# Optimization experiments

Measured on AMD Instinct MI355X. Metric: run time of the kernel, lower is better.

Reference implementation:

```python
import jax, jax.numpy as jnp
import numpy as np

N = 100_000      # nodes
E = 1_600_000    # edges (avg degree 16)
D = 64           # node feature dim
C = 2            # num_classes
K = 2            # propagation hops


def setup_inputs() -> dict:
    key = jax.random.key(0)
    k1, k2, k3 = jax.random.split(key, 3)
    x = jax.random.normal(k1, (N, D), dtype=jnp.float32)
    edge_index = jax.random.randint(k2, (2, E), 0, N, dtype=jnp.int64)
    W = jax.random.normal(k3, (C, D), dtype=jnp.float32) * 0.1  # torch Linear weight [out,in]
    b = jnp.zeros((C,), dtype=jnp.float32)
    return {"x": x, "edge_index": edge_index, "W": W, "b": b}


def reference(x, edge_index, W, b):
    n = x.shape[0]
    self_loop = jnp.arange(n, dtype=edge_index.dtype)
    row = jnp.concatenate([edge_index[0], self_loop])  # source
    col = jnp.concatenate([edge_index[1], self_loop])  # target
    # GCN symmetric normalization with self-loops (PyG gcn_norm)
    deg = jax.ops.segment_sum(jnp.ones(col.shape, dtype=x.dtype), col, num_segments=n)
    dinv = jnp.where(deg > 0, jax.lax.rsqrt(deg), 0.0)
    norm = dinv[row] * dinv[col]                      # [E+N]
    # K-hop propagation: x <- A_hat x
    for _ in range(K):
        x = jax.ops.segment_sum(norm[:, None] * x[row], col, num_segments=n)
    logits = x @ W.T + b                               # [N, C]
    return jax.nn.log_softmax(logits, axis=1)
```

## Files before the change

### kernel.cpp

```cpp
#include <hip/hip_runtime.h>
#include <hip/hip_bf16.h>
#include <math.h>


#define NODES 100000
#define EDGES 1600000
#define DIM 64

#define PBITS 12
#define PSIZE 4096
#define P_BUCKETS 25
#define CAP 131072
#define NSLICE 10
#define PART_BLOCKS 256
#define SEG (EDGES / PART_BLOCKS)
#define PAIRS (SEG / 2)

__global__ void init_kernel(const void* ei, int* mode, int* cursor) {
  int t = threadIdx.x;
  const int* p = (const int*)ei;
  unsigned long long ball = __ballot(p[2 * t + 1] == 0);
  if (t == 0) *mode = (ball == ~0ULL) ? 1 : 0;
  if (t < P_BUCKETS) cursor[t] = t * CAP;
}

__global__ void partition_kernel(const void* ei, const int* __restrict__ mode,
                                 int* __restrict__ cursor,
                                 int2* __restrict__ ecbuf) {
  __shared__ int lcnt[P_BUCKETS];
  __shared__ int lbase[P_BUCKETS];
  int t = threadIdx.x;
  int m = *mode;
  int pbase = blockIdx.x * PAIRS;

  if (t < P_BUCKETS) lcnt[t] = 0;
  __syncthreads();

  if (m) {
    const longlong2* cp =
        (const longlong2*)((const long long*)ei + EDGES) + pbase;
    for (int i = t; i < PAIRS; i += 256) {
      longlong2 v = cp[i];
      atomicAdd(&lcnt[((int)v.x) >> PBITS], 1);
      atomicAdd(&lcnt[((int)v.y) >> PBITS], 1);
    }
  } else {
    const int2* cp = (const int2*)((const int*)ei + EDGES) + pbase;
    for (int i = t; i < PAIRS; i += 256) {
      int2 v = cp[i];
      atomicAdd(&lcnt[v.x >> PBITS], 1);
      atomicAdd(&lcnt[v.y >> PBITS], 1);
    }
  }
  __syncthreads();
  if (t < P_BUCKETS) {
    lbase[t] = atomicAdd(&cursor[t], lcnt[t]);
    lcnt[t] = 0;
  }
  __syncthreads();

  if (m) {
    const longlong2* rp = (const longlong2*)ei + pbase;
    const longlong2* cp =
        (const longlong2*)((const long long*)ei + EDGES) + pbase;
    for (int i = t; i < PAIRS; i += 256) {
      longlong2 rv = rp[i];
      longlong2 cv = cp[i];
      int r0 = (int)rv.x, c0 = (int)cv.x;
      int b0 = c0 >> PBITS;
      int p0 = lbase[b0] + atomicAdd(&lcnt[b0], 1);
      if (p0 < (b0 + 1) * CAP) ecbuf[p0] = make_int2(r0, c0 & (PSIZE - 1));
      int r1 = (int)rv.y, c1 = (int)cv.y;
      int b1 = c1 >> PBITS;
      int p1 = lbase[b1] + atomicAdd(&lcnt[b1], 1);
      if (p1 < (b1 + 1) * CAP) ecbuf[p1] = make_int2(r1, c1 & (PSIZE - 1));
    }
  } else {
    const int2* rp = (const int2*)ei + pbase;
    const int2* cp = (const int2*)((const int*)ei + EDGES) + pbase;
    for (int i = t; i < PAIRS; i += 256) {
      int2 rv = rp[i];
      int2 cv = cp[i];
      int b0 = cv.x >> PBITS;
      int p0 = lbase[b0] + atomicAdd(&lcnt[b0], 1);
      if (p0 < (b0 + 1) * CAP) ecbuf[p0] = make_int2(rv.x, cv.x & (PSIZE - 1));
      int b1 = cv.y >> PBITS;
      int p1 = lbase[b1] + atomicAdd(&lcnt[b1], 1);
      if (p1 < (b1 + 1) * CAP) ecbuf[p1] = make_int2(rv.y, cv.y & (PSIZE - 1));
    }
  }
}

__global__ void deg_kernel(const int* __restrict__ cursor,
                           const int2* __restrict__ ecbuf,
                           float* __restrict__ dinv) {
  __shared__ int h[PSIZE];
  int p = blockIdx.x;
  for (int i = threadIdx.x; i < PSIZE; i += 1024) h[i] = 0;
  __syncthreads();
  int base = p * CAP;
  int cnt = min(cursor[p] - base, CAP);
  for (int e = threadIdx.x; e < cnt; e += 1024)
    atomicAdd(&h[ecbuf[base + e].y], 1);
  __syncthreads();
  int gbase = p << PBITS;
  for (int i = threadIdx.x; i < PSIZE; i += 1024) {
    int g = gbase + i;
    if (g < NODES) dinv[g] = rsqrtf((float)(h[i] + 1));
  }
}

__global__ void proj_kernel(const float* __restrict__ x,
                            const float* __restrict__ W,
                            const float* __restrict__ dinv,
                            float2* __restrict__ ts) {
  int wid = (blockIdx.x * (blockDim.x >> 6)) + (threadIdx.x >> 6);
  int d = threadIdx.x & 63;
  if (wid >= NODES) return;
  float xv = x[(size_t)wid * DIM + d];
  float p0 = xv * W[d];
  float p1 = xv * W[DIM + d];
#pragma unroll
  for (int off = 32; off >= 1; off >>= 1) {
    p0 += __shfl_xor(p0, off, 64);
    p1 += __shfl_xor(p1, off, 64);
  }
  if (d == 0) {
    float di = dinv[wid];
    float2 t;
    t.x = di * p0;
    t.y = di * p1;
    ts[wid] = t;
  }
}

__global__ void hop_kernel(const int* __restrict__ cursor,
                           const int2* __restrict__ ecbuf,
                           const float2* __restrict__ feat,
                           float2* __restrict__ hpart) {
  __shared__ float lx[PSIZE];
  __shared__ float ly[PSIZE];
  int p = blockIdx.x / NSLICE, s = blockIdx.x % NSLICE;
  for (int i = threadIdx.x; i < PSIZE; i += 512) {
    lx[i] = 0.f;
    ly[i] = 0.f;
  }
  __syncthreads();
  int base = p * CAP;
  int cnt = min(cursor[p] - base, CAP);
  int per = (cnt + NSLICE - 1) / NSLICE;
  int beg = base + s * per;
  int end = min(base + cnt, beg + per);
  for (int e = beg + threadIdx.x; e < end; e += 512) {
    int2 ec = ecbuf[e];
    float2 v = feat[ec.x];
    atomicAdd(&lx[ec.y], v.x);
    atomicAdd(&ly[ec.y], v.y);
  }
  __syncthreads();
  float2* outp = hpart + (size_t)blockIdx.x * PSIZE;
  for (int i = threadIdx.x; i < PSIZE; i += 512) {
    float2 o;
    o.x = lx[i];
    o.y = ly[i];
    outp[i] = o;
  }
}

__global__ void merge1_kernel(const float2* __restrict__ hpart,
                              const float2* __restrict__ ts,
                              const float* __restrict__ dinv,
                              float2* __restrict__ z) {
  int i = blockIdx.x * blockDim.x + threadIdx.x;
  if (i >= NODES) return;
  int p = i >> PBITS, l = i & (PSIZE - 1);
  float2 t0 = ts[i];
  float ax = t0.x, ay = t0.y;
#pragma unroll
  for (int s = 0; s < NSLICE; s++) {
    float2 v = hpart[(size_t)(p * NSLICE + s) * PSIZE + l];
    ax += v.x;
    ay += v.y;
  }
  float di = dinv[i];
  float sc = di * di;
  float2 o;
  o.x = sc * ax;
  o.y = sc * ay;
  z[i] = o;
}

__global__ void merge2_kernel(const float2* __restrict__ hpart,
                              const float2* __restrict__ z,
                              const float* __restrict__ dinv,
                              const float* __restrict__ bias,
                              float2* __restrict__ out) {
  int i = blockIdx.x * blockDim.x + threadIdx.x;
  if (i >= NODES) return;
  int p = i >> PBITS, l = i & (PSIZE - 1);
  float2 z0 = z[i];
  float ax = z0.x, ay = z0.y;
#pragma unroll
  for (int s = 0; s < NSLICE; s++) {
    float2 v = hpart[(size_t)(p * NSLICE + s) * PSIZE + l];
    ax += v.x;
    ay += v.y;
  }
  float di = dinv[i];
  float l0 = di * ax + bias[0];
  float l1 = di * ay + bias[1];
  float m = fmaxf(l0, l1);
  float ls = m + logf(expf(l0 - m) + expf(l1 - m));
  float2 o;
  o.x = l0 - ls;
  o.y = l1 - ls;
  out[i] = o;
}

extern "C" void kernel_launch(void* const* d_in, const int* in_sizes, int n_in,
                              void* d_out, int out_size, void* d_ws,
                              size_t ws_size, hipStream_t stream) {
  const float* x = (const float*)d_in[0];
  const void* ei = d_in[1];
  const float* W = (const float*)d_in[2];
  const float* b = (const float*)d_in[3];
  float2* out = (float2*)d_out;

  char* w = (char*)d_ws;
  size_t off = 0;
  auto alloc = [&](size_t bytes) -> char* {
    char* p = w + off;
    off += (bytes + 255) & ~(size_t)255;
    return p;
  };
  int* mode = (int*)alloc(sizeof(int));
  int* cursor = (int*)alloc(P_BUCKETS * sizeof(int));
  int2* ecbuf = (int2*)alloc((size_t)P_BUCKETS * CAP * sizeof(int2));
  float* dinv = (float*)alloc(NODES * sizeof(float));
  float2* ts = (float2*)alloc(NODES * sizeof(float2));
  float2* z = (float2*)alloc(NODES * sizeof(float2));
  float2* hpart =
      (float2*)alloc((size_t)P_BUCKETS * NSLICE * PSIZE * sizeof(float2));
  (void)ws_size;

  const int NGRID = (NODES + 255) / 256;

  init_kernel<<<1, 64, 0, stream>>>(ei, mode, cursor);
  partition_kernel<<<PART_BLOCKS, 256, 0, stream>>>(ei, mode, cursor, ecbuf);
  deg_kernel<<<P_BUCKETS, 1024, 0, stream>>>(cursor, ecbuf, dinv);

  const int WPB = 256 / 64;
  proj_kernel<<<(NODES + WPB - 1) / WPB, 256, 0, stream>>>(x, W, dinv, ts);

  hop_kernel<<<P_BUCKETS * NSLICE, 512, 0, stream>>>(cursor, ecbuf, ts, hpart);
  merge1_kernel<<<NGRID, 256, 0, stream>>>(hpart, ts, dinv, z);
  hop_kernel<<<P_BUCKETS * NSLICE, 512, 0, stream>>>(cursor, ecbuf, z, hpart);
  merge2_kernel<<<NGRID, 256, 0, stream>>>(hpart, z, dinv, b, out);
}
```

Baseline: 177.4 us.

## Fuse GCN pipeline into single cooperative persistent kernel with grid syncs

Replaces the eight separate launches (init, partition, degree, projection, two hops, two merges) with one cooperative kernel of 250 blocks of 1024 threads. The stages are separated by grid-wide syncs. Degree counting is split across slices with a per-slice histogram merge, and the projection uses 16-lane groups with float4 loads. The goal is to remove launch gaps and tail effects between small kernels. The cost is grid-sync overhead, and the partition phase now runs with fewer, larger blocks. The old multi-kernel path is kept as a fallback if the cooperative launch fails.

```diff
diff --git a/kernel.cpp b/kernel.cpp
--- a/kernel.cpp
+++ b/kernel.cpp
@@ -1,6 +1,8 @@
 #include <hip/hip_runtime.h>
-#include <hip/hip_bf16.h>
+#include <hip/hip_cooperative_groups.h>
 #include <math.h>
+
+namespace cg = cooperative_groups;
 
 
 #define NODES 100000
@@ -12,11 +14,209 @@
 #define P_BUCKETS 25
 #define CAP 131072
 #define NSLICE 10
-#define PART_BLOCKS 256
-#define SEG (EDGES / PART_BLOCKS)
-#define PAIRS (SEG / 2)
-
-__global__ void init_kernel(const void* ei, int* mode, int* cursor) {
+#define NBLOCKS (P_BUCKETS * NSLICE)
+#define NT 1024
+#define NPB (NODES / NBLOCKS)
+#define EPB (EDGES / NBLOCKS)
+#define PPB (EPB / 2)
+
+__global__ __launch_bounds__(NT) void gcn_all(
+    const void* __restrict__ ei, const float* __restrict__ x,
+    const float* __restrict__ W, const float* __restrict__ bias,
+    float2* __restrict__ out, int* __restrict__ mode, int* __restrict__ cursor,
+    int2* __restrict__ ecbuf, int* __restrict__ dpart,
+    float* __restrict__ dinv, float2* __restrict__ ts, float2* __restrict__ z,
+    float2* __restrict__ hpart) {
+  cg::grid_group grid = cg::this_grid();
+  __shared__ int shCnt[P_BUCKETS];
+  __shared__ int shBase[P_BUCKETS];
+  __shared__ int shHist[PSIZE];
+  __shared__ float shAx[PSIZE];
+  __shared__ float shAy[PSIZE];
+
+  const int b = blockIdx.x;
+  const int t = threadIdx.x;
+
+  if (b == 0) {
+    if (t < 64) {
+      const int* p = (const int*)ei;
+      unsigned long long ball = __ballot(p[2 * t + 1] == 0);
+      if (t == 0) *mode = (ball == ~0ULL) ? 1 : 0;
+    }
+    if (t < P_BUCKETS) cursor[t] = t * CAP;
+  }
+  grid.sync();
+
+  {
+    const int m = *mode;
+    if (t < P_BUCKETS) shCnt[t] = 0;
+    __syncthreads();
+    const int pbase = b * PPB;
+    if (m) {
+      const longlong2* cp =
+          (const longlong2*)((const long long*)ei + EDGES) + pbase;
+      for (int i = t; i < PPB; i += NT) {
+        longlong2 v = cp[i];
+        atomicAdd(&shCnt[((int)v.x) >> PBITS], 1);
+        atomicAdd(&shCnt[((int)v.y) >> PBITS], 1);
+      }
+    } else {
+      const int2* cp = (const int2*)((const int*)ei + EDGES) + pbase;
+      for (int i = t; i < PPB; i += NT) {
+        int2 v = cp[i];
+        atomicAdd(&shCnt[v.x >> PBITS], 1);
+        atomicAdd(&shCnt[v.y >> PBITS], 1);
+      }
+    }
+    __syncthreads();
+    if (t < P_BUCKETS) {
+      shBase[t] = atomicAdd(&cursor[t], shCnt[t]);
+      shCnt[t] = 0;
+    }
+    __syncthreads();
+    if (m) {
+      const longlong2* rp = (const longlong2*)ei + pbase;
+      const longlong2* cp =
+          (const longlong2*)((const long long*)ei + EDGES) + pbase;
+      for (int i = t; i < PPB; i += NT) {
+        longlong2 rv = rp[i];
+        longlong2 cv = cp[i];
+        int c0 = (int)cv.x, b0 = c0 >> PBITS;
+        int p0 = shBase[b0] + atomicAdd(&shCnt[b0], 1);
+        if (p0 < (b0 + 1) * CAP)
+          ecbuf[p0] = make_int2((int)rv.x, c0 & (PSIZE - 1));
+        int c1 = (int)cv.y, b1 = c1 >> PBITS;
+        int p1 = shBase[b1] + atomicAdd(&shCnt[b1], 1);
+        if (p1 < (b1 + 1) * CAP)
+          ecbuf[p1] = make_int2((int)rv.y, c1 & (PSIZE - 1));
+      }
+    } else {
+      const int2* rp = (const int2*)ei + pbase;
+      const int2* cp = (const int2*)((const int*)ei + EDGES) + pbase;
+      for (int i = t; i < PPB; i += NT) {
+        int2 rv = rp[i];
+        int2 cv = cp[i];
+        int b0 = cv.x >> PBITS;
+        int p0 = shBase[b0] + atomicAdd(&shCnt[b0], 1);
+        if (p0 < (b0 + 1) * CAP)
+          ecbuf[p0] = make_int2(rv.x, cv.x & (PSIZE - 1));
+        int b1 = cv.y >> PBITS;
+        int p1 = shBase[b1] + atomicAdd(&shCnt[b1], 1);
+        if (p1 < (b1 + 1) * CAP)
+          ecbuf[p1] = make_int2(rv.y, cv.y & (PSIZE - 1));
+      }
+    }
+  }
+  grid.sync();
+
+  const int pb = b / NSLICE, sl = b % NSLICE;
+  const int sbase = pb * CAP;
+  const int scnt = min(cursor[pb] - sbase, CAP);
+  const int sper = (scnt + NSLICE - 1) / NSLICE;
+  const int sbeg = sbase + sl * sper;
+  const int send = min(sbase + scnt, sbeg + sper);
+
+  {
+    for (int i = t; i < PSIZE; i += NT) shHist[i] = 0;
+    __syncthreads();
+    for (int e = sbeg + t; e < send; e += NT)
+      atomicAdd(&shHist[ecbuf[e].y], 1);
+    __syncthreads();
+    int* op = dpart + (size_t)b * PSIZE;
+    for (int i = t; i < PSIZE; i += NT) op[i] = shHist[i];
+  }
+  grid.sync();
+
+  {
+    const int nbase = b * NPB;
+    if (t < NPB) {
+      int i = nbase + t;
+      int p = i >> PBITS, l = i & (PSIZE - 1);
+      int d = 0;
+#pragma unroll
+      for (int s = 0; s < NSLICE; s++)
+        d += dpart[(size_t)(p * NSLICE + s) * PSIZE + l];
+      dinv[i] = rsqrtf((float)(d + 1));
+    }
+    __syncthreads();
+    const int wave = t >> 6, lane = t & 63;
+    const int g = lane >> 4, r = lane & 15;
+    for (int k = wave * 4; k < NPB; k += (NT / 64) * 4) {
+      int kk = k + g;
+      if (kk < NPB) {
+        int node = nbase + kk;
+        float4 xv = *(const float4*)&x[(size_t)node * DIM + r * 4];
+        float4 w0 = *(const float4*)&W[r * 4];
+        float4 w1 = *(const float4*)&W[DIM + r * 4];
+        float p0 = xv.x * w0.x + xv.y * w0.y + xv.z * w0.z + xv.w * w0.w;
+        float p1 = xv.x * w1.x + xv.y * w1.y + xv.z * w1.z + xv.w * w1.w;
+#pragma unroll
+        for (int off = 8; off >= 1; off >>= 1) {
+          p0 += __shfl_xor(p0, off, 16);
+          p1 += __shfl_xor(p1, off, 16);
+        }
+        if (r == 0) {
+          float di = dinv[node];
+          ts[node] = make_float2(di * p0, di * p1);
+        }
+      }
+    }
+  }
+  grid.sync();
+
+  for (int hop = 0; hop < 2; ++hop) {
+    const float2* feat = hop ? z : ts;
+    for (int i = t; i < PSIZE; i += NT) {
+      shAx[i] = 0.f;
+      shAy[i] = 0.f;
+    }
+    __syncthreads();
+    for (int e = sbeg + t; e < send; e += NT) {
+      int2 ec = ecbuf[e];
+      float2 v = feat[ec.x];
+      atomicAdd(&shAx[ec.y], v.x);
+      atomicAdd(&shAy[ec.y], v.y);
+    }
+    __syncthreads();
+    {
+      float2* op = hpart + (size_t)b * PSIZE;
+      for (int i = t; i < PSIZE; i += NT)
+        op[i] = make_float2(shAx[i], shAy[i]);
+    }
+    grid.sync();
+    const int nbase = b * NPB;
+    if (t < NPB) {
+      int i = nbase + t;
+      int p = i >> PBITS, l = i & (PSIZE - 1);
+      float2 self = hop ? z[i] : ts[i];
+      float ax = self.x, ay = self.y;
+#pragma unroll
+      for (int s = 0; s < NSLICE; s++) {
+        float2 v = hpart[(size_t)(p * NSLICE + s) * PSIZE + l];
+        ax += v.x;
+        ay += v.y;
+      }
+      float di = dinv[i];
+      if (hop == 0) {
+        float sc = di * di;
+        z[i] = make_float2(sc * ax, sc * ay);
+      } else {
+        float l0 = di * ax + bias[0];
+        float l1 = di * ay + bias[1];
+        float mm = fmaxf(l0, l1);
+        float ls = mm + logf(expf(l0 - mm) + expf(l1 - mm));
+        out[i] = make_float2(l0 - ls, l1 - ls);
+      }
+    }
+    if (hop == 0) grid.sync();
+  }
+}
+
+#define FPART_BLOCKS 256
+#define FSEG (EDGES / FPART_BLOCKS)
+#define FPAIRS (FSEG / 2)
+
+__global__ void fb_init(const void* ei, int* mode, int* cursor) {
   int t = threadIdx.x;
   const int* p = (const int*)ei;
   unsigned long long ball = __ballot(p[2 * t + 1] == 0);
@@ -24,29 +224,25 @@
   if (t < P_BUCKETS) cursor[t] = t * CAP;
 }
 
-__global__ void partition_kernel(const void* ei, const int* __restrict__ mode,
-                                 int* __restrict__ cursor,
-                                 int2* __restrict__ ecbuf) {
+__global__ void fb_partition(const void* ei, const int* __restrict__ mode,
+                             int* __restrict__ cursor, int2* __restrict__ ecbuf) {
   __shared__ int lcnt[P_BUCKETS];
   __shared__ int lbase[P_BUCKETS];
   int t = threadIdx.x;
   int m = *mode;
-  int pbase = blockIdx.x * PAIRS;
-
+  int pbase = blockIdx.x * FPAIRS;
   if (t < P_BUCKETS) lcnt[t] = 0;
   __syncthreads();
-
   if (m) {
-    const longlong2* cp =
-        (const longlong2*)((const long long*)ei + EDGES) + pbase;
-    for (int i = t; i < PAIRS; i += 256) {
+    const longlong2* cp = (const longlong2*)((const long long*)ei + EDGES) + pbase;
+    for (int i = t; i < FPAIRS; i += 256) {
       longlong2 v = cp[i];
       atomicAdd(&lcnt[((int)v.x) >> PBITS], 1);
       atomicAdd(&lcnt[((int)v.y) >> PBITS], 1);
     }
   } else {
     const int2* cp = (const int2*)((const int*)ei + EDGES) + pbase;
-    for (int i = t; i < PAIRS; i += 256) {
+    for (int i = t; i < FPAIRS; i += 256) {
       int2 v = cp[i];
       atomicAdd(&lcnt[v.x >> PBITS], 1);
       atomicAdd(&lcnt[v.y >> PBITS], 1);
@@ -58,27 +254,23 @@
     lcnt[t] = 0;
   }
   __syncthreads();
-
   if (m) {
     const longlong2* rp = (const longlong2*)ei + pbase;
-    const longlong2* cp =
-        (const longlong2*)((const long long*)ei + EDGES) + pbase;
-    for (int i = t; i < PAIRS; i += 256) {
+    const longlong2* cp = (const longlong2*)((const long long*)ei + EDGES) + pbase;
+    for (int i = t; i < FPAIRS; i += 256) {
       longlong2 rv = rp[i];
       longlong2 cv = cp[i];
-      int r0 = (int)rv.x, c0 = (int)cv.x;
-      int b0 = c0 >> PBITS;
+      int c0 = (int)cv.x, b0 = c0 >> PBITS;
       int p0 = lbase[b0] + atomicAdd(&lcnt[b0], 1);
-      if (p0 < (b0 + 1) * CAP) ecbuf[p0] = make_int2(r0, c0 & (PSIZE - 1));
-      int r1 = (int)rv.y, c1 = (int)cv.y;
-      int b1 = c1 >> PBITS;
+      if (p0 < (b0 + 1) * CAP) ecbuf[p0] = make_int2((int)rv.x, c0 & (PSIZE - 1));
+      int c1 = (int)cv.y, b1 = c1 >> PBITS;
       int p1 = lbase[b1] + atomicAdd(&lcnt[b1], 1);
-      if (p1 < (b1 + 1) * CAP) ecbuf[p1] = make_int2(r1, c1 & (PSIZE - 1));
+      if (p1 < (b1 + 1) * CAP) ecbuf[p1] = make_int2((int)rv.y, c1 & (PSIZE - 1));
     }
   } else {
     const int2* rp = (const int2*)ei + pbase;
     const int2* cp = (const int2*)((const int*)ei + EDGES) + pbase;
-    for (int i = t; i < PAIRS; i += 256) {
+    for (int i = t; i < FPAIRS; i += 256) {
       int2 rv = rp[i];
       int2 cv = cp[i];
       int b0 = cv.x >> PBITS;
@@ -91,9 +283,8 @@
   }
 }
 
-__global__ void deg_kernel(const int* __restrict__ cursor,
-                           const int2* __restrict__ ecbuf,
-                           float* __restrict__ dinv) {
+__global__ void fb_deg(const int* __restrict__ cursor,
+                       const int2* __restrict__ ecbuf, float* __restrict__ dinv) {
   __shared__ int h[PSIZE];
   int p = blockIdx.x;
   for (int i = threadIdx.x; i < PSIZE; i += 1024) h[i] = 0;
@@ -110,10 +301,8 @@
   }
 }
 
-__global__ void proj_kernel(const float* __restrict__ x,
-                            const float* __restrict__ W,
-                            const float* __restrict__ dinv,
-                            float2* __restrict__ ts) {
+__global__ void fb_proj(const float* __restrict__ x, const float* __restrict__ W,
+                        const float* __restrict__ dinv, float2* __restrict__ ts) {
   int wid = (blockIdx.x * (blockDim.x >> 6)) + (threadIdx.x >> 6);
   int d = threadIdx.x & 63;
   if (wid >= NODES) return;
@@ -127,17 +316,14 @@
   }
   if (d == 0) {
     float di = dinv[wid];
-    float2 t;
-    t.x = di * p0;
-    t.y = di * p1;
-    ts[wid] = t;
-  }
-}
-
-__global__ void hop_kernel(const int* __restrict__ cursor,
-                           const int2* __restrict__ ecbuf,
-                           const float2* __restrict__ feat,
-                           float2* __restrict__ hpart) {
+    ts[wid] = make_float2(di * p0, di * p1);
+  }
+}
+
+__global__ void fb_hop(const int* __restrict__ cursor,
+                       const int2* __restrict__ ecbuf,
+                       const float2* __restrict__ feat,
+                       float2* __restrict__ hpart) {
   __shared__ float lx[PSIZE];
   __shared__ float ly[PSIZE];
   int p = blockIdx.x / NSLICE, s = blockIdx.x % NSLICE;
@@ -159,18 +345,13 @@
   }
   __syncthreads();
   float2* outp = hpart + (size_t)blockIdx.x * PSIZE;
-  for (int i = threadIdx.x; i < PSIZE; i += 512) {
-    float2 o;
-    o.x = lx[i];
-    o.y = ly[i];
-    outp[i] = o;
-  }
-}
-
-__global__ void merge1_kernel(const float2* __restrict__ hpart,
-                              const float2* __restrict__ ts,
-                              const float* __restrict__ dinv,
-                              float2* __restrict__ z) {
+  for (int i = threadIdx.x; i < PSIZE; i += 512)
+    outp[i] = make_float2(lx[i], ly[i]);
+}
+
+__global__ void fb_merge1(const float2* __restrict__ hpart,
+                          const float2* __restrict__ ts,
+                          const float* __restrict__ dinv, float2* __restrict__ z) {
   int i = blockIdx.x * blockDim.x + threadIdx.x;
   if (i >= NODES) return;
   int p = i >> PBITS, l = i & (PSIZE - 1);
@@ -184,17 +365,14 @@
   }
   float di = dinv[i];
   float sc = di * di;
-  float2 o;
-  o.x = sc * ax;
-  o.y = sc * ay;
-  z[i] = o;
-}
-
-__global__ void merge2_kernel(const float2* __restrict__ hpart,
-                              const float2* __restrict__ z,
-                              const float* __restrict__ dinv,
-                              const float* __restrict__ bias,
-                              float2* __restrict__ out) {
+  z[i] = make_float2(sc * ax, sc * ay);
+}
+
+__global__ void fb_merge2(const float2* __restrict__ hpart,
+                          const float2* __restrict__ z,
+                          const float* __restrict__ dinv,
+                          const float* __restrict__ bias,
+                          float2* __restrict__ out) {
   int i = blockIdx.x * blockDim.x + threadIdx.x;
   if (i >= NODES) return;
   int p = i >> PBITS, l = i & (PSIZE - 1);
@@ -211,19 +389,16 @@
   float l1 = di * ay + bias[1];
   float m = fmaxf(l0, l1);
   float ls = m + logf(expf(l0 - m) + expf(l1 - m));
-  float2 o;
-  o.x = l0 - ls;
-  o.y = l1 - ls;
-  out[i] = o;
+  out[i] = make_float2(l0 - ls, l1 - ls);
 }
 
 extern "C" void kernel_launch(void* const* d_in, const int* in_sizes, int n_in,
                               void* d_out, int out_size, void* d_ws,
                               size_t ws_size, hipStream_t stream) {
+  const void* ei = d_in[1];
   const float* x = (const float*)d_in[0];
-  const void* ei = d_in[1];
   const float* W = (const float*)d_in[2];
-  const float* b = (const float*)d_in[3];
+  const float* bias = (const float*)d_in[3];
   float2* out = (float2*)d_out;
 
   char* w = (char*)d_ws;
@@ -236,24 +411,30 @@
   int* mode = (int*)alloc(sizeof(int));
   int* cursor = (int*)alloc(P_BUCKETS * sizeof(int));
   int2* ecbuf = (int2*)alloc((size_t)P_BUCKETS * CAP * sizeof(int2));
+  int* dpart = (int*)alloc((size_t)NBLOCKS * PSIZE * sizeof(int));
   float* dinv = (float*)alloc(NODES * sizeof(float));
   float2* ts = (float2*)alloc(NODES * sizeof(float2));
   float2* z = (float2*)alloc(NODES * sizeof(float2));
-  float2* hpart =
-      (float2*)alloc((size_t)P_BUCKETS * NSLICE * PSIZE * sizeof(float2));
+  float2* hpart = (float2*)alloc((size_t)NBLOCKS * PSIZE * sizeof(float2));
   (void)ws_size;
 
-  const int NGRID = (NODES + 255) / 256;
-
-  init_kernel<<<1, 64, 0, stream>>>(ei, mode, cursor);
-  partition_kernel<<<PART_BLOCKS, 256, 0, stream>>>(ei, mode, cursor, ecbuf);
-  deg_kernel<<<P_BUCKETS, 1024, 0, stream>>>(cursor, ecbuf, dinv);
-
-  const int WPB = 256 / 64;
-  proj_kernel<<<(NODES + WPB - 1) / WPB, 256, 0, stream>>>(x, W, dinv, ts);
-
-  hop_kernel<<<P_BUCKETS * NSLICE, 512, 0, stream>>>(cursor, ecbuf, ts, hpart);
-  merge1_kernel<<<NGRID, 256, 0, stream>>>(hpart, ts, dinv, z);
-  hop_kernel<<<P_BUCKETS * NSLICE, 512, 0, stream>>>(cursor, ecbuf, z, hpart);
-  merge2_kernel<<<NGRID, 256, 0, stream>>>(hpart, z, dinv, b, out);
-}
+  void* args[] = {(void*)&ei,    (void*)&x,     (void*)&W,     (void*)&bias,
+                  (void*)&out,   (void*)&mode,  (void*)&cursor, (void*)&ecbuf,
+                  (void*)&dpart, (void*)&dinv,  (void*)&ts,     (void*)&z,
+                  (void*)&hpart};
+  hipError_t err = hipLaunchCooperativeKernel(
+      reinterpret_cast<void*>(gcn_all), dim3(NBLOCKS), dim3(NT), args, 0,
+      stream);
+  if (err != hipSuccess) {
+    const int NGRID = (NODES + 255) / 256;
+    fb_init<<<1, 64, 0, stream>>>(ei, mode, cursor);
+    fb_partition<<<FPART_BLOCKS, 256, 0, stream>>>(ei, mode, cursor, ecbuf);
+    fb_deg<<<P_BUCKETS, 1024, 0, stream>>>(cursor, ecbuf, dinv);
+    const int WPB = 256 / 64;
+    fb_proj<<<(NODES + WPB - 1) / WPB, 256, 0, stream>>>(x, W, dinv, ts);
+    fb_hop<<<NBLOCKS, 512, 0, stream>>>(cursor, ecbuf, ts, hpart);
+    fb_merge1<<<NGRID, 256, 0, stream>>>(hpart, ts, dinv, z);
+    fb_hop<<<NBLOCKS, 512, 0, stream>>>(cursor, ecbuf, z, hpart);
+    fb_merge2<<<NGRID, 256, 0, stream>>>(hpart, z, dinv, bias, out);
+  }
+}
```

After: 357.4 us. +101.4%, slower.
